# Kernel optimization log

Measured on AMD Instinct MI355X. Metric: run time of the kernel, lower is better.

## Reference

```python
import jax, jax.numpy as jnp
import numpy as np

IN_FEATURES = 4096
OUT_FEATURES = 4096
BLOCK_SIZE = 64
P = 0.1          # fraction of blocks kept
N_TOKENS = 8192


def setup_inputs() -> dict:
    key = jax.random.key(0)
    k_x, k_w, k_m, k_b = jax.random.split(key, 4)
    x = jax.random.normal(k_x, (N_TOKENS, IN_FEATURES), dtype=jnp.float32)
    # kaiming_uniform_(a=sqrt(5)) on [out, in] -> bound = 1/sqrt(in_features)
    bound = 1.0 / np.sqrt(IN_FEATURES)
    weight = jax.random.uniform(k_w, (OUT_FEATURES, IN_FEATURES), dtype=jnp.float32,
                                minval=-bound, maxval=bound)
    bias = jax.random.uniform(k_b, (OUT_FEATURES,), dtype=jnp.float32,
                              minval=-bound, maxval=bound)
    # Block-structured 0/1 mask: keep each BLOCK_SIZE x BLOCK_SIZE block with prob P
    nb_out, nb_in = OUT_FEATURES // BLOCK_SIZE, IN_FEATURES // BLOCK_SIZE
    block_keep = (jax.random.uniform(k_m, (nb_out, nb_in)) < P).astype(jnp.float32)
    mask = jnp.repeat(jnp.repeat(block_keep, BLOCK_SIZE, axis=0), BLOCK_SIZE, axis=1)
    return {"input": x, "weight": weight, "bias": bias, "mask": mask}


def reference(input, weight, bias, mask):
    # bsr_dense_mm((W*mask).to_sparse_bsr(), x.T).T + bias == x @ (W*mask).T + bias
    masked_w = weight * mask                      # [out, in]
    return input @ masked_w.T + bias              # [N, out]
```

## Files before the change

### kernel.cpp

```cpp
#include <hip/hip_runtime.h>
#include <hip/hip_fp16.h>
#include <cstdint>

#define IN_F   4096
#define OUT_F  4096
#define BS     64
#define NB     64
#define N_TOK  8192
#define TM     256
#define BK     64
#define NMT    (N_TOK / TM)

typedef __attribute__((ext_vector_type(8))) _Float16       f16x8;
typedef __attribute__((ext_vector_type(8))) unsigned short u16x8;
typedef __attribute__((ext_vector_type(4))) float          f32x4;

#define WS_XT_OFF      0ull
#define WS_XT_BYTES    (2048ull * 32768ull)
#define WS_WT_OFF      (WS_XT_OFF + WS_XT_BYTES)
#define WS_WT_BYTES    (4096ull * 8192ull)
#define WS_NEEDED      (WS_WT_OFF + WS_WT_BYTES)

__device__ __forceinline__ u16x8 cvt_f16x8(const float* v) {
    u16x8 o;
#pragma unroll
    for (int j = 0; j < 8; ++j)
        o[j] = __half_as_ushort(__float2half_rn(v[j]));
    return o;
}

__device__ __forceinline__ unsigned long long mask_ballot(
        const float* __restrict__ mask, int br, int lane) {
    float mv = mask[(size_t)(br * BS) * IN_F + (size_t)lane * BS];
    return __ballot(mv != 0.0f);
}

__global__ __launch_bounds__(256)
void convert_all_kernel(const float* __restrict__ x,
                        const float* __restrict__ w,
                        const float* __restrict__ mask,
                        unsigned short* __restrict__ xt,
                        unsigned short* __restrict__ wt) {
    const int b = blockIdx.x;
    if (b < 2048) {
        const int xcd = b & 7;
        const int j   = b >> 3;
        const int mt  = xcd * 4 + (j >> 6);
        const int kb  = j & 63;
        unsigned short* tile = xt + (size_t)(mt * 64 + kb) * 16384;
#pragma unroll
        for (int l = 0; l < 8; ++l) {
            int g    = threadIdx.x + l * 256;
            int row  = g >> 3, slot = g & 7;
            const float* src = x + (size_t)(mt * TM + row) * IN_F + kb * BK + slot * 8;
            float4 v0 = *(const float4*)src;
            float4 v1 = *(const float4*)(src + 4);
            float v[8] = {v0.x, v0.y, v0.z, v0.w, v1.x, v1.y, v1.z, v1.w};
            *(u16x8*)&tile[row * 64 + ((slot ^ (row & 7)) << 3)] = cvt_f16x8(v);
        }
    } else {
        const int wb   = b - 2048;
        const int br   = wb >> 6, si = wb & 63;
        const int lane = threadIdx.x & 63;
        unsigned long long ball = mask_ballot(mask, br, lane);
        if (si >= __popcll(ball)) return;
        bool fl = ((ball >> lane) & 1ull) &&
                  (__popcll(ball & ((1ull << lane) - 1ull)) == si);
        unsigned long long m2 = __ballot(fl);
        const int kb = __ffsll(m2) - 1;
        unsigned short* tile = wt + (size_t)(br * NB + si) * 4096;
#pragma unroll
        for (int l = 0; l < 2; ++l) {
            int g    = threadIdx.x + l * 256;
            int row  = g >> 3, slot = g & 7;
            const float* src = w + (size_t)(br * BS + row) * IN_F + kb * BK + slot * 8;
            float4 v0 = *(const float4*)src;
            float4 v1 = *(const float4*)(src + 4);
            float v[8] = {v0.x, v0.y, v0.z, v0.w, v1.x, v1.y, v1.z, v1.w};
            *(u16x8*)&tile[row * 64 + ((slot ^ (row & 7)) << 3)] = cvt_f16x8(v);
        }
    }
}

__device__ __forceinline__ void gll16(const void* g, void* l) {
    __builtin_amdgcn_global_load_lds(
        (const __attribute__((address_space(1))) unsigned int*)g,
        (__attribute__((address_space(3))) unsigned int*)l, 16, 0, 0);
}

__global__ __launch_bounds__(256, 2)
void bsr_mfma5_kernel(const unsigned short* __restrict__ xt,
                      const unsigned short* __restrict__ wt,
                      const float* __restrict__ bias,
                      const float* __restrict__ mask,
                      float* __restrict__ out) {
    __shared__ unsigned short xs[2][TM * BK];
    __shared__ unsigned short wsb[2][BS * BK];

    const int b     = blockIdx.x;
    const int xcd   = b & 7;
    const int j     = b >> 3;
    const int phase = j >> 7;
    const int idx   = j & 127;
    const int br    = idx >> 1;
    const int mt    = xcd * 4 + phase * 2 + (idx & 1);

    const int tid  = threadIdx.x;
    const int lane = tid & 63;
    const int wv   = tid >> 6;
    const int fr   = lane & 15;
    const int kg   = lane >> 4;

    unsigned long long ball = mask_ballot(mask, br, lane);
    const int cnt = __popcll(ball);

    f32x4 acc[4][4];
#pragma unroll
    for (int a = 0; a < 4; ++a)
#pragma unroll
        for (int c = 0; c < 4; ++c) acc[a][c] = (f32x4)0.0f;

    const char* xbase = (const char*)xt;
    const char* wbase = (const char*)wt;

    auto stage = [&](int kb, int si, int bb) {
        const char* xg = xbase + ((size_t)(mt * 64 + kb) << 15);
        const char* wg = wbase + ((size_t)(br * 64 + si) << 13);
        const int bx = wv * 8192;
#pragma unroll
        for (int q = 0; q < 8; ++q)
            gll16(xg + bx + q * 1024 + lane * 16, (char*)xs[bb] + bx + q * 1024);
        const int bw = wv * 2048;
#pragma unroll
        for (int q = 0; q < 2; ++q)
            gll16(wg + bw + q * 1024 + lane * 16, (char*)wsb[bb] + bw + q * 1024);
    };

    unsigned long long rem = ball;
    int cur = 0;
    if (cnt > 0) {
        int kb0 = __ffsll(rem) - 1;
        rem &= rem - 1;
        stage(kb0, 0, 0);
    }
    __syncthreads();

    for (int si = 0; si < cnt; ++si) {
        if (si + 1 < cnt) {
            int kbn = __ffsll(rem) - 1;
            rem &= rem - 1;
            stage(kbn, si + 1, cur ^ 1);
        }

#pragma unroll
        for (int ks = 0; ks < 2; ++ks) {
            f16x8 a[4], bfr[4];
#pragma unroll
            for (int mr = 0; mr < 4; ++mr) {
                int row = wv * 64 + mr * 16 + fr;
                a[mr] = *(const f16x8*)&xs[cur][row * 64 + (((ks * 4 + kg) ^ (row & 7)) << 3)];
            }
#pragma unroll
            for (int nr = 0; nr < 4; ++nr) {
                int row = nr * 16 + fr;
                bfr[nr] = *(const f16x8*)&wsb[cur][row * 64 + (((ks * 4 + kg) ^ (row & 7)) << 3)];
            }
#pragma unroll
            for (int mr = 0; mr < 4; ++mr)
#pragma unroll
                for (int nr = 0; nr < 4; ++nr)
                    acc[mr][nr] = __builtin_amdgcn_mfma_f32_16x16x32_f16(
                        a[mr], bfr[nr], acc[mr][nr], 0, 0, 0);
        }
        __syncthreads();
        cur ^= 1;
    }

    const int mbase = mt * TM;
    const int obase = br * BS;
#pragma unroll
    for (int nr = 0; nr < 4; ++nr) {
        float bv = bias[obase + nr * 16 + fr];
#pragma unroll
        for (int mr = 0; mr < 4; ++mr) {
#pragma unroll
            for (int r = 0; r < 4; ++r) {
                int m = mbase + wv * 64 + mr * 16 + kg * 4 + r;
                out[(size_t)m * OUT_F + obase + nr * 16 + fr] = acc[mr][nr][r] + bv;
            }
        }
    }
}

__global__ __launch_bounds__(256, 3)
void bsr_fused_kernel(const float* __restrict__ x,
                      const float* __restrict__ w,
                      const float* __restrict__ bias,
                      const float* __restrict__ mask,
                      float* __restrict__ out) {
    __shared__ unsigned short xs[128 * BK];
    __shared__ unsigned short wsb[BS * BK];

    const int mt   = blockIdx.x;
    const int br   = blockIdx.y;
    const int tid  = threadIdx.x;
    const int lane = tid & 63;
    const int wv   = tid >> 6;
    const int fr   = lane & 15;
    const int kg   = lane >> 4;

    const int mbase = mt * 128;
    const int obase = br * BS;

    unsigned long long ball = mask_ballot(mask, br, lane);
    const int cnt = __popcll(ball);
    unsigned long long rem = ball;

    f32x4 acc[2][4];
#pragma unroll
    for (int a = 0; a < 2; ++a)
#pragma unroll
        for (int c = 0; c < 4; ++c) acc[a][c] = (f32x4)0.0f;

    for (int si = 0; si < cnt; ++si) {
        const int kb = __ffsll(rem) - 1;
        rem &= rem - 1;
        const int kbase = kb * BS;
#pragma unroll
        for (int l = 0; l < 4; ++l) {
            int g = tid + l * 256;
            int row = g >> 3, slot = g & 7;
            const float* src = x + (size_t)(mbase + row) * IN_F + kbase + slot * 8;
            float4 v0 = *(const float4*)src;
            float4 v1 = *(const float4*)(src + 4);
            float v[8] = {v0.x, v0.y, v0.z, v0.w, v1.x, v1.y, v1.z, v1.w};
            *(u16x8*)&xs[row * BK + ((slot ^ (row & 7)) << 3)] = cvt_f16x8(v);
        }
#pragma unroll
        for (int l = 0; l < 2; ++l) {
            int g = tid + l * 256;
            int row = g >> 3, slot = g & 7;
            const float* src = w + (size_t)(obase + row) * IN_F + kbase + slot * 8;
            float4 v0 = *(const float4*)src;
            float4 v1 = *(const float4*)(src + 4);
            float v[8] = {v0.x, v0.y, v0.z, v0.w, v1.x, v1.y, v1.z, v1.w};
            *(u16x8*)&wsb[row * BK + ((slot ^ (row & 7)) << 3)] = cvt_f16x8(v);
        }
        __syncthreads();
#pragma unroll
        for (int ks = 0; ks < 2; ++ks) {
            f16x8 a[2], bfr[4];
#pragma unroll
            for (int mr = 0; mr < 2; ++mr) {
                int row = wv * 32 + mr * 16 + fr;
                a[mr] = *(const f16x8*)&xs[row * BK + (((ks * 4 + kg) ^ (row & 7)) << 3)];
            }
#pragma unroll
            for (int nr = 0; nr < 4; ++nr) {
                int row = nr * 16 + fr;
                bfr[nr] = *(const f16x8*)&wsb[row * BK + (((ks * 4 + kg) ^ (row & 7)) << 3)];
            }
#pragma unroll
            for (int mr = 0; mr < 2; ++mr)
#pragma unroll
                for (int nr = 0; nr < 4; ++nr)
                    acc[mr][nr] = __builtin_amdgcn_mfma_f32_16x16x32_f16(
                        a[mr], bfr[nr], acc[mr][nr], 0, 0, 0);
        }
        __syncthreads();
    }

#pragma unroll
    for (int nr = 0; nr < 4; ++nr) {
        float bv = bias[obase + nr * 16 + fr];
#pragma unroll
        for (int mr = 0; mr < 2; ++mr) {
#pragma unroll
            for (int r = 0; r < 4; ++r) {
                int m = mbase + wv * 32 + mr * 16 + kg * 4 + r;
                out[(size_t)m * OUT_F + obase + nr * 16 + fr] = acc[mr][nr][r] + bv;
            }
        }
    }
}

extern "C" void kernel_launch(void* const* d_in, const int* in_sizes, int n_in,
                              void* d_out, int out_size, void* d_ws, size_t ws_size,
                              hipStream_t stream) {
    const float* x    = (const float*)d_in[0];
    const float* w    = (const float*)d_in[1];
    const float* bias = (const float*)d_in[2];
    const float* mask = (const float*)d_in[3];
    float* out = (float*)d_out;

    if (ws_size >= WS_NEEDED) {
        unsigned short* xt = (unsigned short*)((char*)d_ws + WS_XT_OFF);
        unsigned short* wt = (unsigned short*)((char*)d_ws + WS_WT_OFF);
        convert_all_kernel<<<2048 + NB * NB, 256, 0, stream>>>(x, w, mask, xt, wt);
        bsr_mfma5_kernel<<<NMT * NB, 256, 0, stream>>>(xt, wt, bias, mask, out);
    } else {
        dim3 grid(N_TOK / 128, NB);
        bsr_fused_kernel<<<grid, 256, 0, stream>>>(x, w, bias, mask, out);
    }
}
```

Before: 118.1 us.

## Convert x to row-major fp16 and gather swizzled tiles in the GEMM loader

The conversion kernel now writes x as a plain row-major fp16 copy using simple streaming vector loads and stores, instead of pre-tiled and swizzled 256x64 tiles. The GEMM kernel computes per-lane global addresses so that global_load_lds gathers rows from the row-major copy straight into the swizzled LDS layout. This is meant to make the conversion pass cheaper and more coalesced. In exchange, the main kernel's x loads become strided row gathers of 128 bytes per row instead of contiguous 32KB tiles. The weight conversion also separates its loads from its stores to raise memory-level parallelism.

```diff
diff --git a/kernel.cpp b/kernel.cpp
--- a/kernel.cpp
+++ b/kernel.cpp
@@ -8,26 +8,18 @@
 #define NB     64
 #define N_TOK  8192
 #define TM     256
-#define BK     64
 #define NMT    (N_TOK / TM)
 
 typedef __attribute__((ext_vector_type(8))) _Float16       f16x8;
 typedef __attribute__((ext_vector_type(8))) unsigned short u16x8;
+typedef __attribute__((ext_vector_type(4))) unsigned short u16x4;
 typedef __attribute__((ext_vector_type(4))) float          f32x4;
 
-#define WS_XT_OFF      0ull
-#define WS_XT_BYTES    (2048ull * 32768ull)
-#define WS_WT_OFF      (WS_XT_OFF + WS_XT_BYTES)
+#define WS_X16_OFF     0ull
+#define WS_X16_BYTES   ((size_t)N_TOK * IN_F * 2ull)
+#define WS_WT_OFF      (WS_X16_OFF + WS_X16_BYTES)
 #define WS_WT_BYTES    (4096ull * 8192ull)
 #define WS_NEEDED      (WS_WT_OFF + WS_WT_BYTES)
-
-__device__ __forceinline__ u16x8 cvt_f16x8(const float* v) {
-    u16x8 o;
-#pragma unroll
-    for (int j = 0; j < 8; ++j)
-        o[j] = __half_as_ushort(__float2half_rn(v[j]));
-    return o;
-}
 
 __device__ __forceinline__ unsigned long long mask_ballot(
         const float* __restrict__ mask, int br, int lane) {
@@ -35,31 +27,36 @@
     return __ballot(mv != 0.0f);
 }
 
+__device__ __forceinline__ u16x8 pack8(f32x4 a, f32x4 b) {
+    u16x8 o;
+#pragma unroll
+    for (int j = 0; j < 4; ++j) o[j]     = __half_as_ushort(__float2half_rn(a[j]));
+#pragma unroll
+    for (int j = 0; j < 4; ++j) o[4 + j] = __half_as_ushort(__float2half_rn(b[j]));
+    return o;
+}
+
 __global__ __launch_bounds__(256)
 void convert_all_kernel(const float* __restrict__ x,
                         const float* __restrict__ w,
                         const float* __restrict__ mask,
-                        unsigned short* __restrict__ xt,
+                        unsigned short* __restrict__ x16,
                         unsigned short* __restrict__ wt) {
     const int b = blockIdx.x;
-    if (b < 2048) {
-        const int xcd = b & 7;
-        const int j   = b >> 3;
-        const int mt  = xcd * 4 + (j >> 6);
-        const int kb  = j & 63;
-        unsigned short* tile = xt + (size_t)(mt * 64 + kb) * 16384;
-#pragma unroll
-        for (int l = 0; l < 8; ++l) {
-            int g    = threadIdx.x + l * 256;
-            int row  = g >> 3, slot = g & 7;
-            const float* src = x + (size_t)(mt * TM + row) * IN_F + kb * BK + slot * 8;
-            float4 v0 = *(const float4*)src;
-            float4 v1 = *(const float4*)(src + 4);
-            float v[8] = {v0.x, v0.y, v0.z, v0.w, v1.x, v1.y, v1.z, v1.w};
-            *(u16x8*)&tile[row * 64 + ((slot ^ (row & 7)) << 3)] = cvt_f16x8(v);
+    if (b < 4096) {
+        const f32x4* xin = (const f32x4*)x;
+        u16x4* xo = (u16x4*)x16;
+        const size_t base = (size_t)b * 2048 + threadIdx.x;
+#pragma unroll
+        for (int it = 0; it < 8; ++it) {
+            f32x4 v = xin[base + it * 256];
+            u16x4 o;
+#pragma unroll
+            for (int j = 0; j < 4; ++j) o[j] = __half_as_ushort(__float2half_rn(v[j]));
+            xo[base + it * 256] = o;
         }
     } else {
-        const int wb   = b - 2048;
+        const int wb   = b - 4096;
         const int br   = wb >> 6, si = wb & 63;
         const int lane = threadIdx.x & 63;
         unsigned long long ball = mask_ballot(mask, br, lane);
@@ -69,15 +66,22 @@
         unsigned long long m2 = __ballot(fl);
         const int kb = __ffsll(m2) - 1;
         unsigned short* tile = wt + (size_t)(br * NB + si) * 4096;
+
+        f32x4 va[2], vb[2];
 #pragma unroll
         for (int l = 0; l < 2; ++l) {
-            int g    = threadIdx.x + l * 256;
-            int row  = g >> 3, slot = g & 7;
-            const float* src = w + (size_t)(br * BS + row) * IN_F + kb * BK + slot * 8;
-            float4 v0 = *(const float4*)src;
-            float4 v1 = *(const float4*)(src + 4);
-            float v[8] = {v0.x, v0.y, v0.z, v0.w, v1.x, v1.y, v1.z, v1.w};
-            *(u16x8*)&tile[row * 64 + ((slot ^ (row & 7)) << 3)] = cvt_f16x8(v);
+            int g   = threadIdx.x + l * 256;
+            int row = g >> 3, slot = g & 7;
+            const f32x4* src = (const f32x4*)(w + (size_t)(br * BS + row) * IN_F
+                                              + kb * BS + slot * 8);
+            va[l] = src[0];
+            vb[l] = src[1];
+        }
+#pragma unroll
+        for (int l = 0; l < 2; ++l) {
+            int g   = threadIdx.x + l * 256;
+            int row = g >> 3, slot = g & 7;
+            *(u16x8*)&tile[row * 64 + ((slot ^ (row & 7)) << 3)] = pack8(va[l], vb[l]);
         }
     }
 }
@@ -89,13 +93,13 @@
 }
 
 __global__ __launch_bounds__(256, 2)
-void bsr_mfma5_kernel(const unsigned short* __restrict__ xt,
+void bsr_mfma6_kernel(const unsigned short* __restrict__ x16,
                       const unsigned short* __restrict__ wt,
                       const float* __restrict__ bias,
                       const float* __restrict__ mask,
                       float* __restrict__ out) {
-    __shared__ unsigned short xs[2][TM * BK];
-    __shared__ unsigned short wsb[2][BS * BK];
+    __shared__ unsigned short xs[2][TM * BS];
+    __shared__ unsigned short wsb[2][BS * BS];
 
     const int b     = blockIdx.x;
     const int xcd   = b & 7;
@@ -120,16 +124,24 @@
 #pragma unroll
         for (int c = 0; c < 4; ++c) acc[a][c] = (f32x4)0.0f;
 
-    const char* xbase = (const char*)xt;
+    int preA[8];
+#pragma unroll
+    for (int q = 0; q < 8; ++q) {
+        int rl = wv * 64 + q * 8 + (lane >> 3);
+        int s  = (lane & 7) ^ (rl & 7);
+        preA[q] = rl * (IN_F * 2) + s * 16;
+    }
+
+    const char* xslab = (const char*)x16 + (size_t)(mt * TM) * (IN_F * 2);
     const char* wbase = (const char*)wt;
 
     auto stage = [&](int kb, int si, int bb) {
-        const char* xg = xbase + ((size_t)(mt * 64 + kb) << 15);
+        const char* xg = xslab + (size_t)kb * 128;
         const char* wg = wbase + ((size_t)(br * 64 + si) << 13);
-        const int bx = wv * 8192;
+        char* ldsA = (char*)xs[bb] + wv * 8192;
 #pragma unroll
         for (int q = 0; q < 8; ++q)
-            gll16(xg + bx + q * 1024 + lane * 16, (char*)xs[bb] + bx + q * 1024);
+            gll16(xg + preA[q], ldsA + q * 1024);
         const int bw = wv * 2048;
 #pragma unroll
         for (int q = 0; q < 2; ++q)
@@ -198,8 +210,8 @@
                       const float* __restrict__ bias,
                       const float* __restrict__ mask,
                       float* __restrict__ out) {
-    __shared__ unsigned short xs[128 * BK];
-    __shared__ unsigned short wsb[BS * BK];
+    __shared__ unsigned short xs[128 * BS];
+    __shared__ unsigned short wsb[BS * BS];
 
     const int mt   = blockIdx.x;
     const int br   = blockIdx.y;
@@ -230,21 +242,15 @@
         for (int l = 0; l < 4; ++l) {
             int g = tid + l * 256;
             int row = g >> 3, slot = g & 7;
-            const float* src = x + (size_t)(mbase + row) * IN_F + kbase + slot * 8;
-            float4 v0 = *(const float4*)src;
-            float4 v1 = *(const float4*)(src + 4);
-            float v[8] = {v0.x, v0.y, v0.z, v0.w, v1.x, v1.y, v1.z, v1.w};
-            *(u16x8*)&xs[row * BK + ((slot ^ (row & 7)) << 3)] = cvt_f16x8(v);
+            const f32x4* src = (const f32x4*)(x + (size_t)(mbase + row) * IN_F + kbase + slot * 8);
+            *(u16x8*)&xs[row * BS + ((slot ^ (row & 7)) << 3)] = pack8(src[0], src[1]);
         }
 #pragma unroll
         for (int l = 0; l < 2; ++l) {
             int g = tid + l * 256;
             int row = g >> 3, slot = g & 7;
-            const float* src = w + (size_t)(obase + row) * IN_F + kbase + slot * 8;
-            float4 v0 = *(const float4*)src;
-            float4 v1 = *(const float4*)(src + 4);
-            float v[8] = {v0.x, v0.y, v0.z, v0.w, v1.x, v1.y, v1.z, v1.w};
-            *(u16x8*)&wsb[row * BK + ((slot ^ (row & 7)) << 3)] = cvt_f16x8(v);
+            const f32x4* src = (const f32x4*)(w + (size_t)(obase + row) * IN_F + kbase + slot * 8);
+            *(u16x8*)&wsb[row * BS + ((slot ^ (row & 7)) << 3)] = pack8(src[0], src[1]);
         }
         __syncthreads();
 #pragma unroll
@@ -253,12 +259,12 @@
 #pragma unroll
             for (int mr = 0; mr < 2; ++mr) {
                 int row = wv * 32 + mr * 16 + fr;
-                a[mr] = *(const f16x8*)&xs[row * BK + (((ks * 4 + kg) ^ (row & 7)) << 3)];
+                a[mr] = *(const f16x8*)&xs[row * BS + (((ks * 4 + kg) ^ (row & 7)) << 3)];
             }
 #pragma unroll
             for (int nr = 0; nr < 4; ++nr) {
                 int row = nr * 16 + fr;
-                bfr[nr] = *(const f16x8*)&wsb[row * BK + (((ks * 4 + kg) ^ (row & 7)) << 3)];
+                bfr[nr] = *(const f16x8*)&wsb[row * BS + (((ks * 4 + kg) ^ (row & 7)) << 3)];
             }
 #pragma unroll
             for (int mr = 0; mr < 2; ++mr)
@@ -294,10 +300,10 @@
     float* out = (float*)d_out;
 
     if (ws_size >= WS_NEEDED) {
-        unsigned short* xt = (unsigned short*)((char*)d_ws + WS_XT_OFF);
-        unsigned short* wt = (unsigned short*)((char*)d_ws + WS_WT_OFF);
-        convert_all_kernel<<<2048 + NB * NB, 256, 0, stream>>>(x, w, mask, xt, wt);
-        bsr_mfma5_kernel<<<NMT * NB, 256, 0, stream>>>(xt, wt, bias, mask, out);
+        unsigned short* x16 = (unsigned short*)((char*)d_ws + WS_X16_OFF);
+        unsigned short* wt  = (unsigned short*)((char*)d_ws + WS_WT_OFF);
+        convert_all_kernel<<<8192, 256, 0, stream>>>(x, w, mask, x16, wt);
+        bsr_mfma6_kernel<<<NMT * NB, 256, 0, stream>>>(x16, wt, bias, mask, out);
     } else {
         dim3 grid(N_TOK / 128, NB);
         bsr_fused_kernel<<<grid, 256, 0, stream>>>(x, w, bias, mask, out);
```

Result: faster. 110.4 us (-6.5%).
